# Performance work log

Measured on AMD Instinct MI355X. Metric: run time of the kernel, lower is better.

## Reference

```python
import jax, jax.numpy as jnp
import numpy as np

KH = KW = 3
SH = SW = 1
DH = DW = 1

def _same_padding(ih, iw):
    eff_kh = (KH - 1) * DH + 1
    eff_kw = (KW - 1) * DW + 1
    out_h = (ih + SH - 1) // SH
    out_w = (iw + SW - 1) // SW
    pad_h = max((out_h - 1) * SH + eff_kh - ih, 0)
    pad_w = max((out_w - 1) * SW + eff_kw - iw, 0)
    pad_top = pad_h // 2
    pad_bottom = pad_h - pad_top
    pad_left = pad_w // 2
    pad_right = pad_w - pad_left
    return (pad_top, pad_bottom), (pad_left, pad_right)


def setup_inputs() -> dict:
    key = jax.random.key(0)
    k1, k2, k3 = jax.random.split(key, 3)
    N, C, H, Wd = 32, 192, 56, 56
    Cout = 384
    x = jax.random.normal(k1, (N, C, H, Wd), dtype=jnp.float32)
    # linear weight (Cout, C*KH*KW) with unfold ordering (c, kh, kw) -> OIHW kernel
    W = jax.random.normal(k2, (Cout, C, KH, KW), dtype=jnp.float32) * (1.0 / np.sqrt(C * KH * KW))
    b = jax.random.normal(k3, (Cout,), dtype=jnp.float32) * 0.01
    return {"x": x, "W": W, "b": b}


def reference(x, W, b):
    # ConvLayer: F.pad('same') -> nn.Unfold -> Linear -> reshape, which is
    # mathematically a 2D conv with OIHW kernel W (unfold orders features as c,kh,kw).
    _, _, H, Wd = x.shape
    pad_hw = _same_padding(H, Wd)
    out = jax.lax.conv_general_dilated(
        x, W,
        window_strides=(SH, SW),
        padding=pad_hw,
        rhs_dilation=(DH, DW),
        dimension_numbers=("NCHW", "OIHW", "NCHW"),
    )
    return out + b[None, :, None, None]
```

## Files before the change

kernel.cpp:

```cpp
#include <hip/hip_runtime.h>
#include <cstdint>
#include <cstddef>

#define N_IMG 32
#define C_IN 192
#define HW 56
#define SPAT 3136
#define C_OUT 384
#define HP 58
#define KPOS 9
#define KTOT 1728
#define NT 27

#define BM 128
#define BN 256
#define NT_CO 3
#define NT_S  392
#define GRID_MAIN (NT_CO*NT_S)

#define BUF_EL 24576
#define B_BASE 8192

typedef __attribute__((ext_vector_type(8))) short short8;
typedef __attribute__((ext_vector_type(4))) float f32x4;

__device__ __forceinline__ unsigned short f2bf(float f) {
  union { float f; unsigned u; } v; v.f = f;
  unsigned u = v.u;
  unsigned r = (u + 0x7FFFu + ((u >> 16) & 1u)) >> 16;
  return (unsigned short)r;
}

__device__ __forceinline__ void async_load16(const void* gsrc, void* ldst) {
  __builtin_amdgcn_global_load_lds(
      (const __attribute__((address_space(1))) unsigned int*)gsrc,
      (__attribute__((address_space(3))) unsigned int*)ldst,
      16, 0, 0);
}

__device__ __forceinline__ void vm6() { asm volatile("s_waitcnt vmcnt(6)" ::: "memory"); }
__device__ __forceinline__ void vm0() { asm volatile("s_waitcnt vmcnt(0)" ::: "memory"); }

__global__ void pack_w(const float* __restrict__ W, unsigned short* __restrict__ Wp) {
  int idx = blockIdx.x*256 + threadIdx.x;
  if (idx >= C_OUT*KPOS*C_IN) return;
  int c   = idx % C_IN;
  int pos = (idx / C_IN) % KPOS;
  int co  = idx / (C_IN*KPOS);
  float v = W[((size_t)co*C_IN + c)*KPOS + pos];
  Wp[idx] = f2bf(v);
}

__global__ void zero_border(unsigned short* __restrict__ Xp) {
  int idx = blockIdx.x*256 + threadIdx.x;
  if (idx >= N_IMG*228*C_IN) return;
  int c    = idx % C_IN;
  int cell = (idx / C_IN) % 228;
  int n    = idx / (C_IN*228);
  int hh, ww;
  if (cell < 116) { hh = (cell < 58) ? 0 : 57; ww = cell % 58; }
  else { int b2 = cell - 116; ww = (b2 < 56) ? 0 : 57; hh = 1 + (b2 % 56); }
  Xp[(((size_t)n*HP + hh)*HP + ww)*C_IN + c] = 0;
}

__global__ void pack_x(const float* __restrict__ x, unsigned short* __restrict__ Xp) {
  __shared__ float tile[64*57];
  int b  = blockIdx.x;
  int cb = b % 3;
  int h  = (b/3) % HW;
  int n  = b / (3*HW);
  int tid = threadIdx.x;
  const float* src = x + (size_t)n*C_IN*SPAT + (size_t)cb*64*SPAT + h*HW;
  #pragma unroll
  for (int i = 0; i < 14; ++i) {
    int idx = i*256 + tid;
    int c = idx / HW, w = idx % HW;
    tile[c*57 + w] = src[(size_t)c*SPAT + w];
  }
  __syncthreads();
  unsigned short* dst = Xp + (((size_t)n*HP + h + 1)*HP + 1)*C_IN + cb*64;
  #pragma unroll
  for (int i = 0; i < 14; ++i) {
    int idx = i*256 + tid;
    int w = idx / 64, c = idx % 64;
    dst[(size_t)w*C_IN + c] = f2bf(tile[c*57 + w]);
  }
}

__global__ __launch_bounds__(512, 2) void conv_gemm(
    const unsigned short* __restrict__ Wp,
    const unsigned short* __restrict__ Xp,
    const float* __restrict__ bias,
    float* __restrict__ out)
{
  __shared__ __attribute__((aligned(16))) unsigned short lds[3][BUF_EL];

  int bid = blockIdx.x;
  int wg = (bid & 7) * (GRID_MAIN/8) + (bid >> 3);
  int cotile = wg % NT_CO;
  int stile  = wg / NT_CO;

  const int tid   = threadIdx.x;
  const int lane  = tid & 63;
  const int wv    = tid >> 6;
  const int wm    = wv >> 2;
  const int wn    = wv & 3;
  const int lanep = lane & 15;
  const int laneq = lane >> 4;
  const int l3    = lane >> 3;
  const int l7    = lane & 7;
  const int gsl   = (l7 ^ l3) << 3;

  const unsigned short* aSrc0 = Wp + (size_t)(cotile*BM + wv*8      + l3)*KTOT + gsl;
  const unsigned short* aSrc1 = Wp + (size_t)(cotile*BM + (wv+8)*8  + l3)*KTOT + gsl;
  const int aOff0 = wv*512;
  const int aOff1 = (wv+8)*512;

  const unsigned short* bSrc[4];
  int bOff[4];
  #pragma unroll
  for (int i = 0; i < 4; ++i) {
    int cbk = i*8 + wv;
    int rb  = cbk*8 + l3;
    int f   = stile*BN + rb;
    int n   = f / SPAT, sp = f % SPAT;
    bSrc[i] = Xp + (((size_t)n*HP + sp/HW)*HP + sp%HW)*C_IN + gsl;
    bOff[i] = B_BASE + cbk*512;
  }

  const int aRd = (wm*64 + lanep)*64 + ((laneq ^ (lanep & 7)) << 3);
  const int bRd = B_BASE + (wn*64 + lanep)*64 + ((laneq ^ (lanep & 7)) << 3);

  f32x4 acc[4][4];
  #pragma unroll
  for (int mf = 0; mf < 4; ++mf)
    #pragma unroll
    for (int nf = 0; nf < 4; ++nf)
      acc[mf][nf] = (f32x4){0.f, 0.f, 0.f, 0.f};

  auto bOffOf = [](int t) {
    int pos = t / 3;
    int c0  = (t - pos*3) * 64;
    int kh  = pos / 3, kw = pos - kh*3;
    return (kh*HP + kw)*C_IN + c0;
  };

  auto stage = [&](int t, unsigned short* base) {
    const int koff = t*64;
    async_load16(aSrc0 + koff, base + aOff0);
    async_load16(aSrc1 + koff, base + aOff1);
    const int bo = bOffOf(t);
    #pragma unroll
    for (int i = 0; i < 4; ++i)
      async_load16(bSrc[i] + bo, base + bOff[i]);
  };

#define PHASE(LB, STAGE_STMT, VM_STMT, DO_BAR)                              \
  {                                                                         \
    const unsigned short* lb_ = (LB);                                       \
    short8 a0_[4], b0_[4], a1_[4], b1_[4];                                  \
    _Pragma("unroll")                                                       \
    for (int mf = 0; mf < 4; ++mf) a0_[mf] = *(const short8*)&lb_[aRd + mf*1024];        \
    _Pragma("unroll")                                                       \
    for (int nf = 0; nf < 4; ++nf) b0_[nf] = *(const short8*)&lb_[bRd + nf*1024];        \
    _Pragma("unroll")                                                       \
    for (int mf = 0; mf < 4; ++mf) a1_[mf] = *(const short8*)&lb_[(aRd + mf*1024) ^ 32]; \
    _Pragma("unroll")                                                       \
    for (int nf = 0; nf < 4; ++nf) b1_[nf] = *(const short8*)&lb_[(bRd + nf*1024) ^ 32]; \
    STAGE_STMT;                                                             \
    __builtin_amdgcn_s_setprio(1);                                          \
    _Pragma("unroll")                                                       \
    for (int mf = 0; mf < 4; ++mf)                                          \
      _Pragma("unroll")                                                     \
      for (int nf = 0; nf < 4; ++nf)                                        \
        acc[mf][nf] = __builtin_amdgcn_mfma_f32_16x16x32_bf16(              \
            a0_[mf], b0_[nf], acc[mf][nf], 0, 0, 0);                        \
    _Pragma("unroll")                                                       \
    for (int mf = 0; mf < 4; ++mf)                                          \
      _Pragma("unroll")                                                     \
      for (int nf = 0; nf < 4; ++nf)                                        \
        acc[mf][nf] = __builtin_amdgcn_mfma_f32_16x16x32_bf16(              \
            a1_[mf], b1_[nf], acc[mf][nf], 0, 0, 0);                        \
    __builtin_amdgcn_s_setprio(0);                                          \
    VM_STMT;                                                                \
    if (DO_BAR) {                                                           \
      __builtin_amdgcn_s_barrier();                                         \
      __builtin_amdgcn_sched_barrier(0);                                    \
    }                                                                       \
  }

  unsigned short* b0 = &lds[0][0];
  unsigned short* b1 = &lds[1][0];
  unsigned short* b2 = &lds[2][0];

  stage(0, b0);
  stage(1, b1);
  vm6();
  __builtin_amdgcn_s_barrier();
  __builtin_amdgcn_sched_barrier(0);

  for (int t0 = 0; t0 < 24; t0 += 3) {
    PHASE(b0, { stage(t0 + 2, b2); }, vm6(), true);
    PHASE(b1, { stage(t0 + 3, b0); }, vm6(), true);
    PHASE(b2, { stage(t0 + 4, b1); }, vm6(), true);
  }
  PHASE(b0, { stage(26, b2); }, vm6(), true);
  PHASE(b1, {}, vm0(), true);
  PHASE(b2, {}, {}, false);
#undef PHASE

  const int coB = cotile*BM + wm*64;
  const int fB  = stile*BN + wn*64;
  #pragma unroll
  for (int nf = 0; nf < 4; ++nf) {
    int f  = fB + nf*16 + lanep;
    int n  = f / SPAT;
    int sp = f % SPAT;
    float* obase = out + (size_t)n*C_OUT*SPAT + sp;
    #pragma unroll
    for (int mf = 0; mf < 4; ++mf) {
      #pragma unroll
      for (int i = 0; i < 4; ++i) {
        int co = coB + mf*16 + laneq*4 + i;
        obase[(size_t)co*SPAT] = acc[mf][nf][i] + bias[co];
      }
    }
  }
}

__global__ void conv_naive(const float* __restrict__ x, const float* __restrict__ W,
                           const float* __restrict__ bias, float* __restrict__ out) {
  size_t idx = (size_t)blockIdx.x*256 + threadIdx.x;
  if (idx >= (size_t)N_IMG*C_OUT*SPAT) return;
  int s  = idx % SPAT;
  int co = (int)((idx / SPAT) % C_OUT);
  int n  = (int)(idx / ((size_t)SPAT*C_OUT));
  int h = s / HW, w = s % HW;
  float acc = bias[co];
  for (int c = 0; c < C_IN; ++c)
    for (int kh = 0; kh < 3; ++kh) {
      int hh = h + kh - 1;
      if (hh < 0 || hh >= HW) continue;
      for (int kw = 0; kw < 3; ++kw) {
        int ww = w + kw - 1;
        if (ww < 0 || ww >= HW) continue;
        acc += x[(((size_t)n*C_IN + c)*HW + hh)*HW + ww]
             * W[(((size_t)co*C_IN + c)*3 + kh)*3 + kw];
      }
    }
  out[idx] = acc;
}

extern "C" void kernel_launch(void* const* d_in, const int* in_sizes, int n_in,
                              void* d_out, int out_size, void* d_ws, size_t ws_size,
                              hipStream_t stream) {
  const float* x = (const float*)d_in[0];
  const float* W = (const float*)d_in[1];
  const float* b = (const float*)d_in[2];
  float* out = (float*)d_out;

  const size_t WP_ELEMS = (size_t)C_OUT*KPOS*C_IN;
  const size_t XP_ELEMS = (size_t)N_IMG*HP*HP*C_IN;
  const size_t NEED = (WP_ELEMS + XP_ELEMS)*2;

  if (ws_size >= NEED) {
    unsigned short* Wp = (unsigned short*)d_ws;
    unsigned short* Xp = Wp + WP_ELEMS;
    zero_border<<<(N_IMG*228*C_IN + 255)/256, 256, 0, stream>>>(Xp);
    pack_w<<<(int)((WP_ELEMS + 255)/256), 256, 0, stream>>>(W, Wp);
    pack_x<<<N_IMG*HW*3, 256, 0, stream>>>(x, Xp);
    conv_gemm<<<GRID_MAIN, 512, 0, stream>>>(Wp, Xp, b, out);
  } else {
    size_t total = (size_t)N_IMG*C_OUT*SPAT;
    conv_naive<<<(int)((total + 255)/256), 256, 0, stream>>>(x, W, b, out);
  }
}
```

Before: 166.3 us.

## Split K across wave pairs with 64x128 warp tiles and LDS reduction

Changes the warp decomposition so pairs of waves split each 64-wide K chunk in half. Each wave now computes a 64x128 output tile instead of 64x64, which halves A-fragment LDS reads per MFMA. The partial sums from the two waves are combined through LDS in the epilogue. This doubles the accumulator registers to 128 floats per lane, adds an extra reduction pass with two syncthreads, and may cut occupancy under launch_bounds(512,2).

```diff
diff --git a/kernel.cpp b/kernel.cpp
--- a/kernel.cpp
+++ b/kernel.cpp
@@ -40,6 +40,7 @@
 
 __device__ __forceinline__ void vm6() { asm volatile("s_waitcnt vmcnt(6)" ::: "memory"); }
 __device__ __forceinline__ void vm0() { asm volatile("s_waitcnt vmcnt(0)" ::: "memory"); }
+#define SBAR0() __builtin_amdgcn_sched_barrier(0)
 
 __global__ void pack_w(const float* __restrict__ W, unsigned short* __restrict__ Wp) {
   int idx = blockIdx.x*256 + threadIdx.x;
@@ -103,8 +104,9 @@
   const int tid   = threadIdx.x;
   const int lane  = tid & 63;
   const int wv    = tid >> 6;
+  const int ws    = wv & 1;
+  const int wn    = (wv >> 1) & 1;
   const int wm    = wv >> 2;
-  const int wn    = wv & 3;
   const int lanep = lane & 15;
   const int laneq = lane >> 4;
   const int l3    = lane >> 3;
@@ -128,14 +130,15 @@
     bOff[i] = B_BASE + cbk*512;
   }
 
-  const int aRd = (wm*64 + lanep)*64 + ((laneq ^ (lanep & 7)) << 3);
-  const int bRd = B_BASE + (wn*64 + lanep)*64 + ((laneq ^ (lanep & 7)) << 3);
-
-  f32x4 acc[4][4];
+  const int swz = (((laneq ^ (lanep & 7)) << 3) ^ (ws << 5));
+  const int aRd = (wm*64 + lanep)*64 + swz;
+  const int bRd = B_BASE + (wn*128 + lanep)*64 + swz;
+
+  f32x4 acc[4][8];
   #pragma unroll
   for (int mf = 0; mf < 4; ++mf)
     #pragma unroll
-    for (int nf = 0; nf < 4; ++nf)
+    for (int nf = 0; nf < 8; ++nf)
       acc[mf][nf] = (f32x4){0.f, 0.f, 0.f, 0.f};
 
   auto bOffOf = [](int t) {
@@ -158,34 +161,24 @@
 #define PHASE(LB, STAGE_STMT, VM_STMT, DO_BAR)                              \
   {                                                                         \
     const unsigned short* lb_ = (LB);                                       \
-    short8 a0_[4], b0_[4], a1_[4], b1_[4];                                  \
+    short8 av_[4], bv_[8];                                                  \
     _Pragma("unroll")                                                       \
-    for (int mf = 0; mf < 4; ++mf) a0_[mf] = *(const short8*)&lb_[aRd + mf*1024];        \
+    for (int mf = 0; mf < 4; ++mf) av_[mf] = *(const short8*)&lb_[aRd + mf*1024]; \
     _Pragma("unroll")                                                       \
-    for (int nf = 0; nf < 4; ++nf) b0_[nf] = *(const short8*)&lb_[bRd + nf*1024];        \
-    _Pragma("unroll")                                                       \
-    for (int mf = 0; mf < 4; ++mf) a1_[mf] = *(const short8*)&lb_[(aRd + mf*1024) ^ 32]; \
-    _Pragma("unroll")                                                       \
-    for (int nf = 0; nf < 4; ++nf) b1_[nf] = *(const short8*)&lb_[(bRd + nf*1024) ^ 32]; \
+    for (int nf = 0; nf < 8; ++nf) bv_[nf] = *(const short8*)&lb_[bRd + nf*1024]; \
     STAGE_STMT;                                                             \
     __builtin_amdgcn_s_setprio(1);                                          \
     _Pragma("unroll")                                                       \
     for (int mf = 0; mf < 4; ++mf)                                          \
       _Pragma("unroll")                                                     \
-      for (int nf = 0; nf < 4; ++nf)                                        \
+      for (int nf = 0; nf < 8; ++nf)                                        \
         acc[mf][nf] = __builtin_amdgcn_mfma_f32_16x16x32_bf16(              \
-            a0_[mf], b0_[nf], acc[mf][nf], 0, 0, 0);                        \
-    _Pragma("unroll")                                                       \
-    for (int mf = 0; mf < 4; ++mf)                                          \
-      _Pragma("unroll")                                                     \
-      for (int nf = 0; nf < 4; ++nf)                                        \
-        acc[mf][nf] = __builtin_amdgcn_mfma_f32_16x16x32_bf16(              \
-            a1_[mf], b1_[nf], acc[mf][nf], 0, 0, 0);                        \
+            av_[mf], bv_[nf], acc[mf][nf], 0, 0, 0);                        \
     __builtin_amdgcn_s_setprio(0);                                          \
     VM_STMT;                                                                \
     if (DO_BAR) {                                                           \
       __builtin_amdgcn_s_barrier();                                         \
-      __builtin_amdgcn_sched_barrier(0);                                    \
+      SBAR0();                                                              \
     }                                                                       \
   }
 
@@ -197,32 +190,88 @@
   stage(1, b1);
   vm6();
   __builtin_amdgcn_s_barrier();
-  __builtin_amdgcn_sched_barrier(0);
+  SBAR0();
 
   for (int t0 = 0; t0 < 24; t0 += 3) {
-    PHASE(b0, { stage(t0 + 2, b2); }, vm6(), true);
-    PHASE(b1, { stage(t0 + 3, b0); }, vm6(), true);
-    PHASE(b2, { stage(t0 + 4, b1); }, vm6(), true);
-  }
-  PHASE(b0, { stage(26, b2); }, vm6(), true);
-  PHASE(b1, {}, vm0(), true);
-  PHASE(b2, {}, {}, false);
+    PHASE(b0, (stage(t0 + 2, b2)), vm6(), true);
+    PHASE(b1, (stage(t0 + 3, b0)), vm6(), true);
+    PHASE(b2, (stage(t0 + 4, b1)), vm6(), true);
+  }
+  PHASE(b0, (stage(26, b2)), vm6(), true);
+  PHASE(b1, (void)0, vm0(), true);
+  PHASE(b2, (void)0, (void)0, false);
 #undef PHASE
 
-  const int coB = cotile*BM + wm*64;
-  const int fB  = stile*BN + wn*64;
-  #pragma unroll
-  for (int nf = 0; nf < 4; ++nf) {
-    int f  = fB + nf*16 + lanep;
-    int n  = f / SPAT;
-    int sp = f % SPAT;
-    float* obase = out + (size_t)n*C_OUT*SPAT + sp;
-    #pragma unroll
-    for (int mf = 0; mf < 4; ++mf) {
+  __syncthreads();
+  {
+    float* red = (float*)&lds[0][0];
+    const int gbase = (wm*2 + wn)*2*4096;
+    if (ws == 0) {
+      const int gw = gbase + 4096;
       #pragma unroll
-      for (int i = 0; i < 4; ++i) {
-        int co = coB + mf*16 + laneq*4 + i;
-        obase[(size_t)co*SPAT] = acc[mf][nf][i] + bias[co];
+      for (int j = 0; j < 4; ++j) {
+        int c = j*16 + lanep;
+        int rsz = (c & 7) << 3;
+        #pragma unroll
+        for (int mf = 0; mf < 4; ++mf) {
+          int r = (mf*16 + laneq*4) ^ rsz;
+          *(f32x4*)&red[gw + c*64 + r] = acc[mf][4 + j];
+        }
+      }
+    } else {
+      const int gw = gbase;
+      #pragma unroll
+      for (int j = 0; j < 4; ++j) {
+        int c = j*16 + lanep;
+        int rsz = (c & 7) << 3;
+        #pragma unroll
+        for (int mf = 0; mf < 4; ++mf) {
+          int r = (mf*16 + laneq*4) ^ rsz;
+          *(f32x4*)&red[gw + c*64 + r] = acc[mf][j];
+        }
+      }
+    }
+    __syncthreads();
+    const int coB = cotile*BM + wm*64;
+    if (ws == 0) {
+      const int gr = gbase;
+      #pragma unroll
+      for (int j = 0; j < 4; ++j) {
+        int c = j*16 + lanep;
+        int rsz = (c & 7) << 3;
+        int f = stile*BN + wn*128 + j*16 + lanep;
+        int n = f / SPAT, sp = f % SPAT;
+        float* obase = out + (size_t)n*C_OUT*SPAT + sp;
+        #pragma unroll
+        for (int mf = 0; mf < 4; ++mf) {
+          int r = (mf*16 + laneq*4) ^ rsz;
+          f32x4 v = *(const f32x4*)&red[gr + c*64 + r];
+          #pragma unroll
+          for (int i = 0; i < 4; ++i) {
+            int co = coB + mf*16 + laneq*4 + i;
+            obase[(size_t)co*SPAT] = acc[mf][j][i] + v[i] + bias[co];
+          }
+        }
+      }
+    } else {
+      const int gr = gbase + 4096;
+      #pragma unroll
+      for (int j = 0; j < 4; ++j) {
+        int c = j*16 + lanep;
+        int rsz = (c & 7) << 3;
+        int f = stile*BN + wn*128 + (4 + j)*16 + lanep;
+        int n = f / SPAT, sp = f % SPAT;
+        float* obase = out + (size_t)n*C_OUT*SPAT + sp;
+        #pragma unroll
+        for (int mf = 0; mf < 4; ++mf) {
+          int r = (mf*16 + laneq*4) ^ rsz;
+          f32x4 v = *(const f32x4*)&red[gr + c*64 + r];
+          #pragma unroll
+          for (int i = 0; i < 4; ++i) {
+            int co = coB + mf*16 + laneq*4 + i;
+            obase[(size_t)co*SPAT] = acc[mf][4 + j][i] + v[i] + bias[co];
+          }
+        }
       }
     }
   }
@@ -259,7 +308,7 @@
   const float* b = (const float*)d_in[2];
   float* out = (float*)d_out;
 
-  const size_t WP_ELEMS = (size_t)C_OUT*KPOS*C_IN;
+  const size_t WP_ELEMS = (size_t)C_OUT*KTOT;
   const size_t XP_ELEMS = (size_t)N_IMG*HP*HP*C_IN;
   const size_t NEED = (WP_ELEMS + XP_ELEMS)*2;
 
```

Measured after the change: 171.9 us. 3.4% more time.
